# Kernel optimization log

Hardware: AMD Instinct MI355X
Metric: run time of the kernel (lower is better)

The kernel has to match this reference:

```python
import jax, jax.numpy as jnp
import numpy as np

B, C, H, W = 64, 256, 48, 48
NH = 8          # num_heads
DH = C // NH    # per-head dim = 32
DFF = 2 * C     # FFN hidden = 512 (hard-coded d_ffn=feature_dim*2)
M = 64          # base_class_num
EPS_NORM = 1e-5
EPS_LN = 1e-5


def setup_inputs() -> dict:
    key = jax.random.key(0)
    ks = jax.random.split(key, 12)
    s = 0.02
    return {
        "feature": jax.random.normal(ks[0], (B, C, H, W), jnp.float32),
        "base_class_weight": jax.random.normal(ks[1], (M, C), jnp.float32),
        # 1x1-conv projections (weight [out,in], bias [out])
        "wq": jax.random.normal(ks[2], (C, C), jnp.float32) * s,
        "bq": jnp.zeros((C,), jnp.float32),
        "wk": jax.random.normal(ks[3], (C, C), jnp.float32) * s,
        "bk": jnp.zeros((C,), jnp.float32),
        "wv": jax.random.normal(ks[4], (C, C), jnp.float32) * s,
        "bv": jnp.zeros((C,), jnp.float32),
        "wm": jax.random.normal(ks[5], (C, C), jnp.float32) * s,
        "bm": jnp.zeros((C,), jnp.float32),
        # FFN_MLP
        "w1": jax.random.normal(ks[6], (DFF, C), jnp.float32) * s,
        "b1": jnp.zeros((DFF,), jnp.float32),
        "w2": jax.random.normal(ks[7], (C, DFF), jnp.float32) * s,
        "b2": jnp.zeros((C,), jnp.float32),
        "gamma": jnp.ones((C,), jnp.float32),
        "beta": jnp.zeros((C,), jnp.float32),
    }


def reference(feature, base_class_weight, wq, bq, wk, bk, wv, bv, wm, bm,
              w1, b1, w2, b2, gamma, beta):
    b, c, h, w = feature.shape
    n = h * w
    feat_cn = feature.reshape(b, c, n)                 # [B,c,N]  (q input, channel-first)
    feat_nc = feat_cn.transpose(0, 2, 1)               # [B,N,c]  ('feature' var in torch)
    kv_cm = jnp.broadcast_to(base_class_weight.T[None], (b, c, M))  # [B,c,M]

    # 1x1-conv projections then split channels as [dim, heads] (dim outer, per torch view)
    qp = (jnp.einsum('oc,bcn->bon', wq, feat_cn) + bq[None, :, None]).reshape(b, DH, NH, n)
    kp = (jnp.einsum('oc,bcm->bom', wk, kv_cm) + bk[None, :, None]).reshape(b, DH, NH, M)
    vp = (jnp.einsum('oc,bcm->bom', wv, kv_cm) + bv[None, :, None]).reshape(b, DH, NH, M)

    scores = jnp.einsum('bdhn,bdhm->bhnm', qp, kp) / jnp.sqrt(jnp.float32(DH))
    prob = jax.nn.softmax(scores, axis=-1)             # [B,H,N,M]
    x = jnp.einsum('bhnm,bdhm->bdhn', prob, vp)        # [B,dim,H,N]
    merged = jnp.einsum('oc,bcn->bon', wm, x.reshape(b, c, n)) + bm[None, :, None]  # [B,c,N]

    # SFTA cosine re-weighting
    aligned = merged.transpose(0, 2, 1)                # [B,N,c]
    an = aligned / (jnp.linalg.norm(aligned, axis=-1, keepdims=True) + EPS_NORM)
    fn = feat_nc / (jnp.linalg.norm(feat_nc, axis=-1, keepdims=True) + EPS_NORM)
    cos = jnp.sum(an * fn, axis=-1)                    # [B,N]
    out = feat_nc * (cos + 1.0)[:, :, None]            # [B,N,c]

    # FFN_MLP (dropout = identity in eval) + residual + LayerNorm
    h1 = jax.nn.relu(jnp.einsum('bnc,fc->bnf', out, w1) + b1)
    src2 = jnp.einsum('bnf,cf->bnc', h1, w2) + b2
    src = out + src2
    mu = jnp.mean(src, axis=-1, keepdims=True)
    var = jnp.mean(jnp.square(src - mu), axis=-1, keepdims=True)
    src = (src - mu) / jnp.sqrt(var + EPS_LN) * gamma + beta

    return src.transpose(0, 2, 1).reshape(b, c, h, w)
```

## Files before the change

### kernel.cpp

```cpp
#include <hip/hip_runtime.h>

#define Bc   64
#define Cc   256
#define Nn   2304
#define DFFf 512
#define Mm   64
#define NTILE 64
#define NTB   36

typedef __bf16 bf16_t;
typedef __bf16 bf16x8 __attribute__((ext_vector_type(8)));
typedef __bf16 bf16x4 __attribute__((ext_vector_type(4)));
typedef float  f32x4  __attribute__((ext_vector_type(4)));

__device__ __forceinline__ bf16_t cvt(float f) { return (bf16_t)f; }

__device__ __forceinline__ f32x4 mfma16(bf16x8 a, bf16x8 b, f32x4 c) {
    return __builtin_amdgcn_mfma_f32_16x16x32_bf16(a, b, c, 0, 0, 0);
}

__global__ void kv_kernel(const float* __restrict__ wk, const float* __restrict__ bk,
                          const float* __restrict__ wv, const float* __restrict__ bv,
                          const float* __restrict__ bcw,
                          float* __restrict__ Kout, float* __restrict__ Vout) {
    int c = blockIdx.x;
    int m = threadIdx.x;
    const float* wkr = wk + c * Cc;
    const float* wvr = wv + c * Cc;
    const float* br  = bcw + m * Cc;
    float aK = 0.f, aV = 0.f;
    #pragma unroll 8
    for (int i = 0; i < Cc; ++i) {
        float bcv = br[i];
        aK = fmaf(wkr[i], bcv, aK);
        aV = fmaf(wvr[i], bcv, aV);
    }
    Kout[c * Mm + m] = aK + bk[c];
    Vout[c * Mm + m] = aV + bv[c];
}

__global__ void pack_kernel(const float* __restrict__ wq, const float* __restrict__ bq,
                            const float* __restrict__ wm, const float* __restrict__ w1,
                            const float* __restrict__ w2,
                            const float* __restrict__ Kf32, const float* __restrict__ Vf32,
                            bf16_t* __restrict__ wqf, bf16_t* __restrict__ wmf,
                            bf16_t* __restrict__ w1f, bf16_t* __restrict__ w2f,
                            bf16_t* __restrict__ Kf, bf16_t* __restrict__ Vf,
                            float* __restrict__ bqp) {
    int idx = blockIdx.x * 256 + threadIdx.x;
    if (idx < 65536) {
        int e = idx;
        int j = e & 7, lane = (e >> 3) & 63, rs = e >> 9;
        int ks = rs & 7, rt = rs >> 3;
        int op = rt * 16 + (lane & 15);
        int k  = ks * 32 + (lane >> 4) * 8 + j;
        int c  = (op & 31) * 8 + (op >> 5);
        wqf[e] = cvt(wq[c * 256 + k]);
    } else if (idx < 131072) {
        int e = idx - 65536;
        int j = e & 7, lane = (e >> 3) & 63, rs = e >> 9;
        int ks = rs & 7, rt = rs >> 3;
        int o = rt * 16 + (lane & 15);
        int k = ks * 32 + (lane >> 4) * 8 + j;
        int c = (k & 31) * 8 + (k >> 5);
        wmf[e] = cvt(wm[o * 256 + c]);
    } else if (idx < 262144) {
        int e = idx - 131072;
        int j = e & 7, lane = (e >> 3) & 63, rs = e >> 9;
        int ks = rs & 7, rt = rs >> 3;
        w1f[e] = cvt(w1[(rt * 16 + (lane & 15)) * 256 + ks * 32 + (lane >> 4) * 8 + j]);
    } else if (idx < 393216) {
        int e = idx - 262144;
        int j = e & 7, lane = (e >> 3) & 63, rs = e >> 9;
        int ks = rs & 15, rt = rs >> 4;
        w2f[e] = cvt(w2[(rt * 16 + (lane & 15)) * 512 + ks * 32 + (lane >> 4) * 8 + j]);
    } else if (idx < 409600) {
        int e = idx - 393216;
        int j = e & 7, lane = (e >> 3) & 63, hm = e >> 9;
        int mt = hm & 3, h = hm >> 2;
        int d = (lane >> 4) * 8 + j, m = mt * 16 + (lane & 15);
        Kf[e] = cvt(Kf32[(d * 8 + h) * 64 + m]);
    } else if (idx < 425984) {
        int e = idx - 409600;
        int j = e & 7, lane = (e >> 3) & 63, x = e >> 9;
        int ks = x & 1, rt = (x >> 1) & 1, h = x >> 2;
        int d = rt * 16 + (lane & 15), m = ks * 32 + (lane >> 4) * 8 + j;
        Vf[e] = cvt(Vf32[(d * 8 + h) * 64 + m]);
    } else if (idx < 426240) {
        int op = idx - 425984;
        int c = (op & 31) * 8 + (op >> 5);
        bqp[op] = bq[c];
    }
}

__global__ __launch_bounds__(256, 2) void sfta_mfma(
    const float* __restrict__ feat,
    const bf16_t* __restrict__ wqf, const float* __restrict__ bqp,
    const bf16_t* __restrict__ wmf, const float* __restrict__ bm,
    const bf16_t* __restrict__ w1f, const float* __restrict__ b1,
    const bf16_t* __restrict__ w2f, const float* __restrict__ b2,
    const bf16_t* __restrict__ Kf,  const bf16_t* __restrict__ Vf,
    const float* __restrict__ gam,  const float* __restrict__ bet,
    float* __restrict__ out) {
    __shared__ __align__(16) bf16_t sFeat[64 * 264];
    __shared__ __align__(16) bf16_t sQX[64 * 264];
    __shared__ __align__(16) bf16_t sP[4][16 * 72];
    __shared__ float sRed[3][4][64];

    const int t    = threadIdx.x;
    const int wid  = t >> 6;
    const int lane = t & 63;
    const int quad = lane >> 4;
    const int lid  = lane & 15;
    const int b    = blockIdx.y;
    const int n0   = blockIdx.x * NTILE;
    const size_t baseF = (size_t)b * Cc * Nn + n0;
    const int rbase = wid * 4;

    {
        int cb = t >> 4;
        int nb = (t & 15) * 4;
        for (int i = 0; i < 16; ++i) {
            int c = i * 16 + cb;
            const float4 f4 = *(const float4*)(feat + baseF + (size_t)c * Nn + nb);
            sFeat[(nb + 0) * 264 + c] = cvt(f4.x);
            sFeat[(nb + 1) * 264 + c] = cvt(f4.y);
            sFeat[(nb + 2) * 264 + c] = cvt(f4.z);
            sFeat[(nb + 3) * 264 + c] = cvt(f4.w);
        }
    }
    __syncthreads();

    bf16_t* pw = sP[wid];

    {
        f32x4 acc[4][4];
        #pragma unroll
        for (int rt = 0; rt < 4; ++rt)
            #pragma unroll
            for (int nt = 0; nt < 4; ++nt) acc[rt][nt] = (f32x4){0.f, 0.f, 0.f, 0.f};
        #pragma unroll
        for (int ks = 0; ks < 8; ++ks) {
            bf16x8 bfr[4];
            #pragma unroll
            for (int nt = 0; nt < 4; ++nt)
                bfr[nt] = *(const bf16x8*)(sFeat + (nt * 16 + lid) * 264 + ks * 32 + quad * 8);
            #pragma unroll
            for (int rt = 0; rt < 4; ++rt) {
                bf16x8 a = *(const bf16x8*)(wqf + (((rbase + rt) * 8 + ks) * 64 + lane) * 8);
                #pragma unroll
                for (int nt = 0; nt < 4; ++nt) acc[rt][nt] = mfma16(a, bfr[nt], acc[rt][nt]);
            }
        }
        #pragma unroll
        for (int rt = 0; rt < 4; ++rt) {
            int ob = (rbase + rt) * 16 + quad * 4;
            #pragma unroll
            for (int nt = 0; nt < 4; ++nt) {
                bf16x4 o;
                #pragma unroll
                for (int r = 0; r < 4; ++r) o[r] = cvt(acc[rt][nt][r] + bqp[ob + r]);
                *(bf16x4*)(sQX + (nt * 16 + lid) * 264 + ob) = o;
            }
        }
    }

    const float scl = 0.17677669529663687f;
    #pragma unroll 1
    for (int hh = 0; hh < 2; ++hh) {
        const int h = wid * 2 + hh;
        bf16x8 kb[4], va[4];
        #pragma unroll
        for (int mt = 0; mt < 4; ++mt)
            kb[mt] = *(const bf16x8*)(Kf + ((h * 4 + mt) * 64 + lane) * 8);
        #pragma unroll
        for (int rv = 0; rv < 4; ++rv)
            va[rv] = *(const bf16x8*)(Vf + ((h * 4 + rv) * 64 + lane) * 8);
        #pragma unroll 1
        for (int g = 0; g < 4; ++g) {
            bf16x8 aq = *(const bf16x8*)(sQX + (g * 16 + lid) * 264 + h * 32 + quad * 8);
            f32x4 sc[4];
            #pragma unroll
            for (int mt = 0; mt < 4; ++mt) {
                f32x4 z = {0.f, 0.f, 0.f, 0.f};
                sc[mt] = mfma16(aq, kb[mt], z);
            }
            float p[4][4];
            #pragma unroll
            for (int r = 0; r < 4; ++r) {
                float v0 = sc[0][r] * scl, v1 = sc[1][r] * scl;
                float v2 = sc[2][r] * scl, v3 = sc[3][r] * scl;
                float mx = fmaxf(fmaxf(v0, v1), fmaxf(v2, v3));
                mx = fmaxf(mx, __shfl_xor(mx, 1));
                mx = fmaxf(mx, __shfl_xor(mx, 2));
                mx = fmaxf(mx, __shfl_xor(mx, 4));
                mx = fmaxf(mx, __shfl_xor(mx, 8));
                v0 = __expf(v0 - mx); v1 = __expf(v1 - mx);
                v2 = __expf(v2 - mx); v3 = __expf(v3 - mx);
                float s = v0 + v1 + v2 + v3;
                s += __shfl_xor(s, 1); s += __shfl_xor(s, 2);
                s += __shfl_xor(s, 4); s += __shfl_xor(s, 8);
                float inv = 1.f / s;
                p[0][r] = v0 * inv; p[1][r] = v1 * inv;
                p[2][r] = v2 * inv; p[3][r] = v3 * inv;
            }
            #pragma unroll
            for (int mt = 0; mt < 4; ++mt)
                #pragma unroll
                for (int r = 0; r < 4; ++r)
                    pw[(quad * 4 + r) * 72 + mt * 16 + lid] = cvt(p[mt][r]);
            #pragma unroll
            for (int rt = 0; rt < 2; ++rt) {
                f32x4 x = {0.f, 0.f, 0.f, 0.f};
                #pragma unroll
                for (int ks = 0; ks < 2; ++ks) {
                    bf16x8 bp = *(const bf16x8*)(pw + lid * 72 + ks * 32 + quad * 8);
                    x = mfma16(va[rt * 2 + ks], bp, x);
                }
                int ob = h * 32 + rt * 16 + quad * 4;
                bf16x4 o;
                #pragma unroll
                for (int r = 0; r < 4; ++r) o[r] = cvt(x[r]);
                *(bf16x4*)(sQX + (g * 16 + lid) * 264 + ob) = o;
            }
        }
    }
    __syncthreads();

    float pmf[4], pmm[4], pff[4];
    {
        f32x4 acc[4][4];
        #pragma unroll
        for (int rt = 0; rt < 4; ++rt)
            #pragma unroll
            for (int nt = 0; nt < 4; ++nt) acc[rt][nt] = (f32x4){0.f, 0.f, 0.f, 0.f};
        #pragma unroll
        for (int ks = 0; ks < 8; ++ks) {
            bf16x8 bx[4];
            #pragma unroll
            for (int nt = 0; nt < 4; ++nt)
                bx[nt] = *(const bf16x8*)(sQX + (nt * 16 + lid) * 264 + ks * 32 + quad * 8);
            #pragma unroll
            for (int rt = 0; rt < 4; ++rt) {
                bf16x8 a = *(const bf16x8*)(wmf + (((rbase + rt) * 8 + ks) * 64 + lane) * 8);
                #pragma unroll
                for (int nt = 0; nt < 4; ++nt) acc[rt][nt] = mfma16(a, bx[nt], acc[rt][nt]);
            }
        }
        #pragma unroll
        for (int nt = 0; nt < 4; ++nt) { pmf[nt] = 0.f; pmm[nt] = 0.f; pff[nt] = 0.f; }
        #pragma unroll
        for (int rt = 0; rt < 4; ++rt) {
            int ob = (rbase + rt) * 16 + quad * 4;
            #pragma unroll
            for (int nt = 0; nt < 4; ++nt) {
                bf16x4 f4 = *(const bf16x4*)(sFeat + (nt * 16 + lid) * 264 + ob);
                #pragma unroll
                for (int r = 0; r < 4; ++r) {
                    float m = acc[rt][nt][r] + bm[ob + r];
                    float f = (float)f4[r];
                    pmf[nt] = fmaf(m, f, pmf[nt]);
                    pmm[nt] = fmaf(m, m, pmm[nt]);
                    pff[nt] = fmaf(f, f, pff[nt]);
                }
            }
        }
    }
    #pragma unroll
    for (int nt = 0; nt < 4; ++nt) {
        pmf[nt] += __shfl_xor(pmf[nt], 16); pmf[nt] += __shfl_xor(pmf[nt], 32);
        pmm[nt] += __shfl_xor(pmm[nt], 16); pmm[nt] += __shfl_xor(pmm[nt], 32);
        pff[nt] += __shfl_xor(pff[nt], 16); pff[nt] += __shfl_xor(pff[nt], 32);
    }
    if (lane < 16) {
        #pragma unroll
        for (int nt = 0; nt < 4; ++nt) {
            sRed[0][wid][nt * 16 + lane] = pmf[nt];
            sRed[1][wid][nt * 16 + lane] = pmm[nt];
            sRed[2][wid][nt * 16 + lane] = pff[nt];
        }
    }
    __syncthreads();

    {
        int row = wid * 16 + lid;
        float smf = sRed[0][0][row] + sRed[0][1][row] + sRed[0][2][row] + sRed[0][3][row];
        float smm = sRed[1][0][row] + sRed[1][1][row] + sRed[1][2][row] + sRed[1][3][row];
        float sff = sRed[2][0][row] + sRed[2][1][row] + sRed[2][2][row] + sRed[2][3][row];
        float scale = smf / ((sqrtf(smm) + 1e-5f) * (sqrtf(sff) + 1e-5f)) + 1.f;
        bf16_t* frow = sFeat + row * 264;
        #pragma unroll
        for (int i = 0; i < 8; ++i) {
            bf16x8* pp = (bf16x8*)(frow + quad * 64 + i * 8);
            bf16x8 v = *pp;
            #pragma unroll
            for (int e = 0; e < 8; ++e) v[e] = cvt((float)v[e] * scale);
            *pp = v;
        }
    }
    __syncthreads();

    f32x4 acc2[4][4];
    #pragma unroll
    for (int rt = 0; rt < 4; ++rt)
        #pragma unroll
        for (int nt = 0; nt < 4; ++nt) acc2[rt][nt] = (f32x4){0.f, 0.f, 0.f, 0.f};
    #pragma unroll 1
    for (int c = 0; c < 2; ++c) {
        f32x4 a1[4][4];
        #pragma unroll
        for (int rtl = 0; rtl < 4; ++rtl)
            #pragma unroll
            for (int nt = 0; nt < 4; ++nt) a1[rtl][nt] = (f32x4){0.f, 0.f, 0.f, 0.f};
        #pragma unroll
        for (int ks = 0; ks < 8; ++ks) {
            bf16x8 bfr[4];
            #pragma unroll
            for (int nt = 0; nt < 4; ++nt)
                bfr[nt] = *(const bf16x8*)(sFeat + (nt * 16 + lid) * 264 + ks * 32 + quad * 8);
            #pragma unroll
            for (int rtl = 0; rtl < 4; ++rtl) {
                int rt1 = c * 16 + rbase + rtl;
                bf16x8 a = *(const bf16x8*)(w1f + ((rt1 * 8 + ks) * 64 + lane) * 8);
                #pragma unroll
                for (int nt = 0; nt < 4; ++nt) a1[rtl][nt] = mfma16(a, bfr[nt], a1[rtl][nt]);
            }
        }
        #pragma unroll
        for (int rtl = 0; rtl < 4; ++rtl) {
            int fb = (c * 16 + rbase + rtl) * 16 + quad * 4;
            int fl = (rbase + rtl) * 16 + quad * 4;
            #pragma unroll
            for (int nt = 0; nt < 4; ++nt) {
                bf16x4 o;
                #pragma unroll
                for (int r = 0; r < 4; ++r) o[r] = cvt(fmaxf(a1[rtl][nt][r] + b1[fb + r], 0.f));
                *(bf16x4*)(sQX + (nt * 16 + lid) * 264 + fl) = o;
            }
        }
        __syncthreads();
        #pragma unroll
        for (int kk = 0; kk < 8; ++kk) {
            bf16x8 bh[4];
            #pragma unroll
            for (int nt = 0; nt < 4; ++nt)
                bh[nt] = *(const bf16x8*)(sQX + (nt * 16 + lid) * 264 + kk * 32 + quad * 8);
            #pragma unroll
            for (int rt = 0; rt < 4; ++rt) {
                bf16x8 a = *(const bf16x8*)(w2f + (((rbase + rt) * 16 + c * 8 + kk) * 64 + lane) * 8);
                #pragma unroll
                for (int nt = 0; nt < 4; ++nt) acc2[rt][nt] = mfma16(a, bh[nt], acc2[rt][nt]);
            }
        }
        __syncthreads();
    }

    float ps[4] = {0.f, 0.f, 0.f, 0.f}, pq[4] = {0.f, 0.f, 0.f, 0.f};
    #pragma unroll
    for (int rt = 0; rt < 4; ++rt) {
        int ob = (rbase + rt) * 16 + quad * 4;
        #pragma unroll
        for (int nt = 0; nt < 4; ++nt) {
            bf16x4 f4 = *(const bf16x4*)(sFeat + (nt * 16 + lid) * 264 + ob);
            #pragma unroll
            for (int r = 0; r < 4; ++r) {
                float v = acc2[rt][nt][r] + b2[ob + r] + (float)f4[r];
                acc2[rt][nt][r] = v;
                ps[nt] += v;
                pq[nt] = fmaf(v, v, pq[nt]);
            }
        }
    }
    #pragma unroll
    for (int nt = 0; nt < 4; ++nt) {
        ps[nt] += __shfl_xor(ps[nt], 16); ps[nt] += __shfl_xor(ps[nt], 32);
        pq[nt] += __shfl_xor(pq[nt], 16); pq[nt] += __shfl_xor(pq[nt], 32);
    }
    if (lane < 16) {
        #pragma unroll
        for (int nt = 0; nt < 4; ++nt) {
            sRed[0][wid][nt * 16 + lane] = ps[nt];
            sRed[1][wid][nt * 16 + lane] = pq[nt];
        }
    }
    __syncthreads();

    float* op = out + baseF;
    #pragma unroll
    for (int nt = 0; nt < 4; ++nt) {
        int row = nt * 16 + lid;
        float s = sRed[0][0][row] + sRed[0][1][row] + sRed[0][2][row] + sRed[0][3][row];
        float q = sRed[1][0][row] + sRed[1][1][row] + sRed[1][2][row] + sRed[1][3][row];
        float mu   = s * (1.f / 256.f);
        float rstd = rsqrtf(q * (1.f / 256.f) - mu * mu + 1e-5f);
        #pragma unroll
        for (int rt = 0; rt < 4; ++rt) {
            int ob = (rbase + rt) * 16 + quad * 4;
            #pragma unroll
            for (int r = 0; r < 4; ++r) {
                float y = (acc2[rt][nt][r] - mu) * rstd * gam[ob + r] + bet[ob + r];
                op[(size_t)(ob + r) * Nn + row] = y;
            }
        }
    }
}

extern "C" void kernel_launch(void* const* d_in, const int* in_sizes, int n_in,
                              void* d_out, int out_size, void* d_ws, size_t ws_size,
                              hipStream_t stream) {
    const float* feature = (const float*)d_in[0];
    const float* bcw     = (const float*)d_in[1];
    const float* wq = (const float*)d_in[2];  const float* bq = (const float*)d_in[3];
    const float* wk = (const float*)d_in[4];  const float* bk = (const float*)d_in[5];
    const float* wv = (const float*)d_in[6];  const float* bv = (const float*)d_in[7];
    const float* wm = (const float*)d_in[8];  const float* bm = (const float*)d_in[9];
    const float* w1 = (const float*)d_in[10]; const float* b1 = (const float*)d_in[11];
    const float* w2 = (const float*)d_in[12]; const float* b2 = (const float*)d_in[13];
    const float* gm = (const float*)d_in[14]; const float* bt = (const float*)d_in[15];

    float*  Kf32 = (float*)d_ws;
    float*  Vf32 = Kf32 + 16384;
    bf16_t* wqf  = (bf16_t*)(Vf32 + 16384);
    bf16_t* wmf  = wqf + 65536;
    bf16_t* w1f  = wmf + 65536;
    bf16_t* w2f  = w1f + 131072;
    bf16_t* Kf   = w2f + 131072;
    bf16_t* Vf   = Kf + 16384;
    float*  bqp  = (float*)(Vf + 16384);

    float* op = (float*)d_out;

    hipLaunchKernelGGL(kv_kernel, dim3(Cc), dim3(Mm), 0, stream,
                       wk, bk, wv, bv, bcw, Kf32, Vf32);
    hipLaunchKernelGGL(pack_kernel, dim3((426240 + 255) / 256), dim3(256), 0, stream,
                       wq, bq, wm, w1, w2, Kf32, Vf32,
                       wqf, wmf, w1f, w2f, Kf, Vf, bqp);
    hipLaunchKernelGGL(sfta_mfma, dim3(NTB, Bc), dim3(256), 0, stream,
                       feature, wqf, bqp, wmf, bm, w1f, b1, w2f, b2,
                       Kf, Vf, gm, bt, op);
}
```

Measured before the change: 510.1 us.

## Use 512-thread blocks with one head per wave and register-resident attention

The fused kernel now runs 8 waves per block instead of 4, so each wave owns 2 output row tiles and exactly one head. The Q weights and K layouts are re-packed so each wave's Q projection result lands directly in MFMA operand registers. Scores are computed as K·Q so the softmax reduces across lanes with two shuffles, and probabilities feed the PV MFMA from registers without the shared-memory P staging buffer. Bias, gamma and beta loads are vectorized, and exp2 with a prescaled factor replaces exp. The risks are higher register and LDS pressure per block under the new launch bounds, and a different accumulation order in the softmax.

```diff
diff --git a/kernel.cpp b/kernel.cpp
--- a/kernel.cpp
+++ b/kernel.cpp
@@ -52,9 +52,11 @@
         int e = idx;
         int j = e & 7, lane = (e >> 3) & 63, rs = e >> 9;
         int ks = rs & 7, rt = rs >> 3;
-        int op = rt * 16 + (lane & 15);
+        int rho = lane & 15;
+        int h = rt >> 1, rtl = rt & 1;
+        int d = 8 * (rho >> 2) + 4 * rtl + (rho & 3);
         int k  = ks * 32 + (lane >> 4) * 8 + j;
-        int c  = (op & 31) * 8 + (op >> 5);
+        int c  = d * 8 + h;
         wqf[e] = cvt(wq[c * 256 + k]);
     } else if (idx < 131072) {
         int e = idx - 65536;
@@ -78,7 +80,9 @@
         int e = idx - 393216;
         int j = e & 7, lane = (e >> 3) & 63, hm = e >> 9;
         int mt = hm & 3, h = hm >> 2;
-        int d = (lane >> 4) * 8 + j, m = mt * 16 + (lane & 15);
+        int lid = lane & 15;
+        int d = (lane >> 4) * 8 + j;
+        int m = 32 * (mt >> 1) + 4 * (mt & 1) + 8 * (lid >> 2) + (lid & 3);
         Kf[e] = cvt(Kf32[(d * 8 + h) * 64 + m]);
     } else if (idx < 425984) {
         int e = idx - 409600;
@@ -93,7 +97,7 @@
     }
 }
 
-__global__ __launch_bounds__(256, 2) void sfta_mfma(
+__global__ __launch_bounds__(512, 4) void sfta_mfma(
     const float* __restrict__ feat,
     const bf16_t* __restrict__ wqf, const float* __restrict__ bqp,
     const bf16_t* __restrict__ wmf, const float* __restrict__ bm,
@@ -104,8 +108,7 @@
     float* __restrict__ out) {
     __shared__ __align__(16) bf16_t sFeat[64 * 264];
     __shared__ __align__(16) bf16_t sQX[64 * 264];
-    __shared__ __align__(16) bf16_t sP[4][16 * 72];
-    __shared__ float sRed[3][4][64];
+    __shared__ float sRed[3][8][64];
 
     const int t    = threadIdx.x;
     const int wid  = t >> 6;
@@ -115,13 +118,13 @@
     const int b    = blockIdx.y;
     const int n0   = blockIdx.x * NTILE;
     const size_t baseF = (size_t)b * Cc * Nn + n0;
-    const int rbase = wid * 4;
 
     {
         int cb = t >> 4;
         int nb = (t & 15) * 4;
-        for (int i = 0; i < 16; ++i) {
-            int c = i * 16 + cb;
+        #pragma unroll
+        for (int i = 0; i < 8; ++i) {
+            int c = i * 32 + cb;
             const float4 f4 = *(const float4*)(feat + baseF + (size_t)c * Nn + nb);
             sFeat[(nb + 0) * 264 + c] = cvt(f4.x);
             sFeat[(nb + 1) * 264 + c] = cvt(f4.y);
@@ -131,14 +134,13 @@
     }
     __syncthreads();
 
-    bf16_t* pw = sP[wid];
-
-    {
-        f32x4 acc[4][4];
-        #pragma unroll
-        for (int rt = 0; rt < 4; ++rt)
-            #pragma unroll
-            for (int nt = 0; nt < 4; ++nt) acc[rt][nt] = (f32x4){0.f, 0.f, 0.f, 0.f};
+    bf16x8 bq[4];
+    {
+        f32x4 qacc[2][4];
+        #pragma unroll
+        for (int rtl = 0; rtl < 2; ++rtl)
+            #pragma unroll
+            for (int nt = 0; nt < 4; ++nt) qacc[rtl][nt] = (f32x4){0.f, 0.f, 0.f, 0.f};
         #pragma unroll
         for (int ks = 0; ks < 8; ++ks) {
             bf16x8 bfr[4];
@@ -146,94 +148,87 @@
             for (int nt = 0; nt < 4; ++nt)
                 bfr[nt] = *(const bf16x8*)(sFeat + (nt * 16 + lid) * 264 + ks * 32 + quad * 8);
             #pragma unroll
-            for (int rt = 0; rt < 4; ++rt) {
-                bf16x8 a = *(const bf16x8*)(wqf + (((rbase + rt) * 8 + ks) * 64 + lane) * 8);
-                #pragma unroll
-                for (int nt = 0; nt < 4; ++nt) acc[rt][nt] = mfma16(a, bfr[nt], acc[rt][nt]);
-            }
-        }
-        #pragma unroll
-        for (int rt = 0; rt < 4; ++rt) {
-            int ob = (rbase + rt) * 16 + quad * 4;
-            #pragma unroll
-            for (int nt = 0; nt < 4; ++nt) {
-                bf16x4 o;
-                #pragma unroll
-                for (int r = 0; r < 4; ++r) o[r] = cvt(acc[rt][nt][r] + bqp[ob + r]);
-                *(bf16x4*)(sQX + (nt * 16 + lid) * 264 + ob) = o;
-            }
-        }
-    }
-
-    const float scl = 0.17677669529663687f;
-    #pragma unroll 1
-    for (int hh = 0; hh < 2; ++hh) {
-        const int h = wid * 2 + hh;
+            for (int rtl = 0; rtl < 2; ++rtl) {
+                bf16x8 a = *(const bf16x8*)(wqf + (((wid * 2 + rtl) * 8 + ks) * 64 + lane) * 8);
+                #pragma unroll
+                for (int nt = 0; nt < 4; ++nt) qacc[rtl][nt] = mfma16(a, bfr[nt], qacc[rtl][nt]);
+            }
+        }
+        const float4 qbA = *(const float4*)(bqp + wid * 32 + quad * 8);
+        const float4 qbB = *(const float4*)(bqp + wid * 32 + quad * 8 + 4);
+        #pragma unroll
+        for (int g = 0; g < 4; ++g) {
+            bq[g][0] = cvt(qacc[0][g][0] + qbA.x);
+            bq[g][1] = cvt(qacc[0][g][1] + qbA.y);
+            bq[g][2] = cvt(qacc[0][g][2] + qbA.z);
+            bq[g][3] = cvt(qacc[0][g][3] + qbA.w);
+            bq[g][4] = cvt(qacc[1][g][0] + qbB.x);
+            bq[g][5] = cvt(qacc[1][g][1] + qbB.y);
+            bq[g][6] = cvt(qacc[1][g][2] + qbB.z);
+            bq[g][7] = cvt(qacc[1][g][3] + qbB.w);
+        }
+    }
+
+    {
         bf16x8 kb[4], va[4];
         #pragma unroll
         for (int mt = 0; mt < 4; ++mt)
-            kb[mt] = *(const bf16x8*)(Kf + ((h * 4 + mt) * 64 + lane) * 8);
+            kb[mt] = *(const bf16x8*)(Kf + ((wid * 4 + mt) * 64 + lane) * 8);
         #pragma unroll
         for (int rv = 0; rv < 4; ++rv)
-            va[rv] = *(const bf16x8*)(Vf + ((h * 4 + rv) * 64 + lane) * 8);
+            va[rv] = *(const bf16x8*)(Vf + ((wid * 4 + rv) * 64 + lane) * 8);
+        const float scl2 = 0.17677669529663687f * 1.4426950408889634f;
         #pragma unroll 1
         for (int g = 0; g < 4; ++g) {
-            bf16x8 aq = *(const bf16x8*)(sQX + (g * 16 + lid) * 264 + h * 32 + quad * 8);
             f32x4 sc[4];
             #pragma unroll
             for (int mt = 0; mt < 4; ++mt) {
                 f32x4 z = {0.f, 0.f, 0.f, 0.f};
-                sc[mt] = mfma16(aq, kb[mt], z);
-            }
-            float p[4][4];
-            #pragma unroll
-            for (int r = 0; r < 4; ++r) {
-                float v0 = sc[0][r] * scl, v1 = sc[1][r] * scl;
-                float v2 = sc[2][r] * scl, v3 = sc[3][r] * scl;
-                float mx = fmaxf(fmaxf(v0, v1), fmaxf(v2, v3));
-                mx = fmaxf(mx, __shfl_xor(mx, 1));
-                mx = fmaxf(mx, __shfl_xor(mx, 2));
-                mx = fmaxf(mx, __shfl_xor(mx, 4));
-                mx = fmaxf(mx, __shfl_xor(mx, 8));
-                v0 = __expf(v0 - mx); v1 = __expf(v1 - mx);
-                v2 = __expf(v2 - mx); v3 = __expf(v3 - mx);
-                float s = v0 + v1 + v2 + v3;
-                s += __shfl_xor(s, 1); s += __shfl_xor(s, 2);
-                s += __shfl_xor(s, 4); s += __shfl_xor(s, 8);
-                float inv = 1.f / s;
-                p[0][r] = v0 * inv; p[1][r] = v1 * inv;
-                p[2][r] = v2 * inv; p[3][r] = v3 * inv;
-            }
+                sc[mt] = mfma16(kb[mt], bq[g], z);
+            }
+            float f[16];
             #pragma unroll
             for (int mt = 0; mt < 4; ++mt)
                 #pragma unroll
-                for (int r = 0; r < 4; ++r)
-                    pw[(quad * 4 + r) * 72 + mt * 16 + lid] = cvt(p[mt][r]);
-            #pragma unroll
-            for (int rt = 0; rt < 2; ++rt) {
+                for (int r = 0; r < 4; ++r) f[mt * 4 + r] = sc[mt][r] * scl2;
+            float mx = f[0];
+            #pragma unroll
+            for (int i = 1; i < 16; ++i) mx = fmaxf(mx, f[i]);
+            mx = fmaxf(mx, __shfl_xor(mx, 16));
+            mx = fmaxf(mx, __shfl_xor(mx, 32));
+            float s = 0.f;
+            #pragma unroll
+            for (int i = 0; i < 16; ++i) { f[i] = exp2f(f[i] - mx); s += f[i]; }
+            s += __shfl_xor(s, 16);
+            s += __shfl_xor(s, 32);
+            float inv = 1.f / s;
+            bf16x8 bp[2];
+            #pragma unroll
+            for (int ks = 0; ks < 2; ++ks)
+                #pragma unroll
+                for (int jj = 0; jj < 8; ++jj)
+                    bp[ks][jj] = cvt(f[(2 * ks + (jj >> 2)) * 4 + (jj & 3)] * inv);
+            #pragma unroll
+            for (int rv = 0; rv < 2; ++rv) {
                 f32x4 x = {0.f, 0.f, 0.f, 0.f};
-                #pragma unroll
-                for (int ks = 0; ks < 2; ++ks) {
-                    bf16x8 bp = *(const bf16x8*)(pw + lid * 72 + ks * 32 + quad * 8);
-                    x = mfma16(va[rt * 2 + ks], bp, x);
-                }
-                int ob = h * 32 + rt * 16 + quad * 4;
+                x = mfma16(va[rv * 2 + 0], bp[0], x);
+                x = mfma16(va[rv * 2 + 1], bp[1], x);
                 bf16x4 o;
                 #pragma unroll
                 for (int r = 0; r < 4; ++r) o[r] = cvt(x[r]);
-                *(bf16x4*)(sQX + (g * 16 + lid) * 264 + ob) = o;
+                *(bf16x4*)(sQX + (g * 16 + lid) * 264 + wid * 32 + rv * 16 + quad * 4) = o;
             }
         }
     }
     __syncthreads();
 
+    f32x4 acc2[2][4];
     float pmf[4], pmm[4], pff[4];
     {
-        f32x4 acc[4][4];
-        #pragma unroll
-        for (int rt = 0; rt < 4; ++rt)
-            #pragma unroll
-            for (int nt = 0; nt < 4; ++nt) acc[rt][nt] = (f32x4){0.f, 0.f, 0.f, 0.f};
+        #pragma unroll
+        for (int rtl = 0; rtl < 2; ++rtl)
+            #pragma unroll
+            for (int nt = 0; nt < 4; ++nt) acc2[rtl][nt] = (f32x4){0.f, 0.f, 0.f, 0.f};
         #pragma unroll
         for (int ks = 0; ks < 8; ++ks) {
             bf16x8 bx[4];
@@ -241,23 +236,26 @@
             for (int nt = 0; nt < 4; ++nt)
                 bx[nt] = *(const bf16x8*)(sQX + (nt * 16 + lid) * 264 + ks * 32 + quad * 8);
             #pragma unroll
-            for (int rt = 0; rt < 4; ++rt) {
-                bf16x8 a = *(const bf16x8*)(wmf + (((rbase + rt) * 8 + ks) * 64 + lane) * 8);
-                #pragma unroll
-                for (int nt = 0; nt < 4; ++nt) acc[rt][nt] = mfma16(a, bx[nt], acc[rt][nt]);
-            }
-        }
+            for (int rtl = 0; rtl < 2; ++rtl) {
+                bf16x8 a = *(const bf16x8*)(wmf + (((wid * 2 + rtl) * 8 + ks) * 64 + lane) * 8);
+                #pragma unroll
+                for (int nt = 0; nt < 4; ++nt) acc2[rtl][nt] = mfma16(a, bx[nt], acc2[rtl][nt]);
+            }
+        }
+        float4 bmv[2];
+        bmv[0] = *(const float4*)(bm + (wid * 2 + 0) * 16 + quad * 4);
+        bmv[1] = *(const float4*)(bm + (wid * 2 + 1) * 16 + quad * 4);
         #pragma unroll
         for (int nt = 0; nt < 4; ++nt) { pmf[nt] = 0.f; pmm[nt] = 0.f; pff[nt] = 0.f; }
         #pragma unroll
-        for (int rt = 0; rt < 4; ++rt) {
-            int ob = (rbase + rt) * 16 + quad * 4;
+        for (int rtl = 0; rtl < 2; ++rtl) {
+            int ob = (wid * 2 + rtl) * 16 + quad * 4;
             #pragma unroll
             for (int nt = 0; nt < 4; ++nt) {
                 bf16x4 f4 = *(const bf16x4*)(sFeat + (nt * 16 + lid) * 264 + ob);
                 #pragma unroll
                 for (int r = 0; r < 4; ++r) {
-                    float m = acc[rt][nt][r] + bm[ob + r];
+                    float m = acc2[rtl][nt][r] + bmv[rtl][r];
                     float f = (float)f4[r];
                     pmf[nt] = fmaf(m, f, pmf[nt]);
                     pmm[nt] = fmaf(m, m, pmm[nt]);
@@ -283,15 +281,20 @@
     __syncthreads();
 
     {
-        int row = wid * 16 + lid;
-        float smf = sRed[0][0][row] + sRed[0][1][row] + sRed[0][2][row] + sRed[0][3][row];
-        float smm = sRed[1][0][row] + sRed[1][1][row] + sRed[1][2][row] + sRed[1][3][row];
-        float sff = sRed[2][0][row] + sRed[2][1][row] + sRed[2][2][row] + sRed[2][3][row];
+        int row = wid * 8 + (lane >> 3);
+        int c0  = (lane & 7) * 32;
+        float smf = 0.f, smm = 0.f, sff = 0.f;
+        #pragma unroll
+        for (int k = 0; k < 8; ++k) {
+            smf += sRed[0][k][row];
+            smm += sRed[1][k][row];
+            sff += sRed[2][k][row];
+        }
         float scale = smf / ((sqrtf(smm) + 1e-5f) * (sqrtf(sff) + 1e-5f)) + 1.f;
-        bf16_t* frow = sFeat + row * 264;
-        #pragma unroll
-        for (int i = 0; i < 8; ++i) {
-            bf16x8* pp = (bf16x8*)(frow + quad * 64 + i * 8);
+        bf16_t* frow = sFeat + row * 264 + c0;
+        #pragma unroll
+        for (int i = 0; i < 4; ++i) {
+            bf16x8* pp = (bf16x8*)(frow + i * 8);
             bf16x8 v = *pp;
             #pragma unroll
             for (int e = 0; e < 8; ++e) v[e] = cvt((float)v[e] * scale);
@@ -300,16 +303,15 @@
     }
     __syncthreads();
 
-    f32x4 acc2[4][4];
     #pragma unroll
-    for (int rt = 0; rt < 4; ++rt)
-        #pragma unroll
-        for (int nt = 0; nt < 4; ++nt) acc2[rt][nt] = (f32x4){0.f, 0.f, 0.f, 0.f};
+    for (int rtl = 0; rtl < 2; ++rtl)
+        #pragma unroll
+        for (int nt = 0; nt < 4; ++nt) acc2[rtl][nt] = (f32x4){0.f, 0.f, 0.f, 0.f};
     #pragma unroll 1
     for (int c = 0; c < 2; ++c) {
-        f32x4 a1[4][4];
-        #pragma unroll
-        for (int rtl = 0; rtl < 4; ++rtl)
+        f32x4 a1[2][4];
+        #pragma unroll
+        for (int rtl = 0; rtl < 2; ++rtl)
             #pragma unroll
             for (int nt = 0; nt < 4; ++nt) a1[rtl][nt] = (f32x4){0.f, 0.f, 0.f, 0.f};
         #pragma unroll
@@ -319,22 +321,25 @@
             for (int nt = 0; nt < 4; ++nt)
                 bfr[nt] = *(const bf16x8*)(sFeat + (nt * 16 + lid) * 264 + ks * 32 + quad * 8);
             #pragma unroll
-            for (int rtl = 0; rtl < 4; ++rtl) {
-                int rt1 = c * 16 + rbase + rtl;
+            for (int rtl = 0; rtl < 2; ++rtl) {
+                int rt1 = c * 16 + wid * 2 + rtl;
                 bf16x8 a = *(const bf16x8*)(w1f + ((rt1 * 8 + ks) * 64 + lane) * 8);
                 #pragma unroll
                 for (int nt = 0; nt < 4; ++nt) a1[rtl][nt] = mfma16(a, bfr[nt], a1[rtl][nt]);
             }
         }
         #pragma unroll
-        for (int rtl = 0; rtl < 4; ++rtl) {
-            int fb = (c * 16 + rbase + rtl) * 16 + quad * 4;
-            int fl = (rbase + rtl) * 16 + quad * 4;
+        for (int rtl = 0; rtl < 2; ++rtl) {
+            int rt1 = c * 16 + wid * 2 + rtl;
+            const float4 b1v = *(const float4*)(b1 + rt1 * 16 + quad * 4);
+            int fl = (wid * 2 + rtl) * 16 + quad * 4;
             #pragma unroll
             for (int nt = 0; nt < 4; ++nt) {
                 bf16x4 o;
-                #pragma unroll
-                for (int r = 0; r < 4; ++r) o[r] = cvt(fmaxf(a1[rtl][nt][r] + b1[fb + r], 0.f));
+                o[0] = cvt(fmaxf(a1[rtl][nt][0] + b1v.x, 0.f));
+                o[1] = cvt(fmaxf(a1[rtl][nt][1] + b1v.y, 0.f));
+                o[2] = cvt(fmaxf(a1[rtl][nt][2] + b1v.z, 0.f));
+                o[3] = cvt(fmaxf(a1[rtl][nt][3] + b1v.w, 0.f));
                 *(bf16x4*)(sQX + (nt * 16 + lid) * 264 + fl) = o;
             }
         }
@@ -346,28 +351,33 @@
             for (int nt = 0; nt < 4; ++nt)
                 bh[nt] = *(const bf16x8*)(sQX + (nt * 16 + lid) * 264 + kk * 32 + quad * 8);
             #pragma unroll
-            for (int rt = 0; rt < 4; ++rt) {
-                bf16x8 a = *(const bf16x8*)(w2f + (((rbase + rt) * 16 + c * 8 + kk) * 64 + lane) * 8);
-                #pragma unroll
-                for (int nt = 0; nt < 4; ++nt) acc2[rt][nt] = mfma16(a, bh[nt], acc2[rt][nt]);
+            for (int rtl = 0; rtl < 2; ++rtl) {
+                bf16x8 a = *(const bf16x8*)(w2f + (((wid * 2 + rtl) * 16 + c * 8 + kk) * 64 + lane) * 8);
+                #pragma unroll
+                for (int nt = 0; nt < 4; ++nt) acc2[rtl][nt] = mfma16(a, bh[nt], acc2[rtl][nt]);
             }
         }
         __syncthreads();
     }
 
     float ps[4] = {0.f, 0.f, 0.f, 0.f}, pq[4] = {0.f, 0.f, 0.f, 0.f};
-    #pragma unroll
-    for (int rt = 0; rt < 4; ++rt) {
-        int ob = (rbase + rt) * 16 + quad * 4;
-        #pragma unroll
-        for (int nt = 0; nt < 4; ++nt) {
-            bf16x4 f4 = *(const bf16x4*)(sFeat + (nt * 16 + lid) * 264 + ob);
-            #pragma unroll
-            for (int r = 0; r < 4; ++r) {
-                float v = acc2[rt][nt][r] + b2[ob + r] + (float)f4[r];
-                acc2[rt][nt][r] = v;
-                ps[nt] += v;
-                pq[nt] = fmaf(v, v, pq[nt]);
+    {
+        float4 b2v[2];
+        b2v[0] = *(const float4*)(b2 + (wid * 2 + 0) * 16 + quad * 4);
+        b2v[1] = *(const float4*)(b2 + (wid * 2 + 1) * 16 + quad * 4);
+        #pragma unroll
+        for (int rtl = 0; rtl < 2; ++rtl) {
+            int ob = (wid * 2 + rtl) * 16 + quad * 4;
+            #pragma unroll
+            for (int nt = 0; nt < 4; ++nt) {
+                bf16x4 f4 = *(const bf16x4*)(sFeat + (nt * 16 + lid) * 264 + ob);
+                #pragma unroll
+                for (int r = 0; r < 4; ++r) {
+                    float v = acc2[rtl][nt][r] + ((const float*)&b2v[rtl])[r] + (float)f4[r];
+                    acc2[rtl][nt][r] = v;
+                    ps[nt] += v;
+                    pq[nt] = fmaf(v, v, pq[nt]);
+                }
             }
         }
     }
@@ -386,19 +396,26 @@
     __syncthreads();
 
     float* op = out + baseF;
+    float4 gv[2], bv[2];
+    gv[0] = *(const float4*)(gam + (wid * 2 + 0) * 16 + quad * 4);
+    gv[1] = *(const float4*)(gam + (wid * 2 + 1) * 16 + quad * 4);
+    bv[0] = *(const float4*)(bet + (wid * 2 + 0) * 16 + quad * 4);
+    bv[1] = *(const float4*)(bet + (wid * 2 + 1) * 16 + quad * 4);
     #pragma unroll
     for (int nt = 0; nt < 4; ++nt) {
         int row = nt * 16 + lid;
-        float s = sRed[0][0][row] + sRed[0][1][row] + sRed[0][2][row] + sRed[0][3][row];
-        float q = sRed[1][0][row] + sRed[1][1][row] + sRed[1][2][row] + sRed[1][3][row];
+        float s = 0.f, q = 0.f;
+        #pragma unroll
+        for (int k = 0; k < 8; ++k) { s += sRed[0][k][row]; q += sRed[1][k][row]; }
         float mu   = s * (1.f / 256.f);
         float rstd = rsqrtf(q * (1.f / 256.f) - mu * mu + 1e-5f);
         #pragma unroll
-        for (int rt = 0; rt < 4; ++rt) {
-            int ob = (rbase + rt) * 16 + quad * 4;
+        for (int rtl = 0; rtl < 2; ++rtl) {
+            int ob = (wid * 2 + rtl) * 16 + quad * 4;
             #pragma unroll
             for (int r = 0; r < 4; ++r) {
-                float y = (acc2[rt][nt][r] - mu) * rstd * gam[ob + r] + bet[ob + r];
+                float y = (acc2[rtl][nt][r] - mu) * rstd * ((const float*)&gv[rtl])[r]
+                          + ((const float*)&bv[rtl])[r];
                 op[(size_t)(ob + r) * Nn + row] = y;
             }
         }
@@ -435,7 +452,7 @@
     hipLaunchKernelGGL(pack_kernel, dim3((426240 + 255) / 256), dim3(256), 0, stream,
                        wq, bq, wm, w1, w2, Kf32, Vf32,
                        wqf, wmf, w1f, w2f, Kf, Vf, bqp);
-    hipLaunchKernelGGL(sfta_mfma, dim3(NTB, Bc), dim3(256), 0, stream,
+    hipLaunchKernelGGL(sfta_mfma, dim3(NTB, Bc), dim3(512), 0, stream,
                        feature, wqf, bqp, wmf, bm, w1f, b1, w2f, b2,
                        Kf, Vf, gm, bt, op);
 }
```

New measurement: 488.7 us. 4.2% less time.
